# Kernel optimization log

Hardware: AMD Instinct MI355X
Metric: run time of the kernel (lower is better)

Reference implementation:

```python
import jax, jax.numpy as jnp
import numpy as np


def setup_inputs() -> dict:
    key = jax.random.key(0)
    ks = jax.random.split(key, 14)
    N, D, H, L, K = 16384, 1024, 1024, 256, 4096
    s = 0.02  # small init scale for stable activations
    return {
        "x": jax.random.uniform(ks[0], (N, D), dtype=jnp.float32),
        "embed_pool": jax.random.normal(ks[1], (K, L), dtype=jnp.float32),
        "ew1": jax.random.normal(ks[2], (D, H), dtype=jnp.float32) * s,
        "eb1": jnp.zeros((H,), jnp.float32),
        "ew2": jax.random.normal(ks[3], (H, H), dtype=jnp.float32) * s,
        "eb2": jnp.zeros((H,), jnp.float32),
        "ew3": jax.random.normal(ks[4], (H, L), dtype=jnp.float32) * s,
        "eb3": jnp.zeros((L,), jnp.float32),
        "dw1": jax.random.normal(ks[5], (L, H), dtype=jnp.float32) * s,
        "db1": jnp.zeros((H,), jnp.float32),
        "dw2": jax.random.normal(ks[6], (H, H), dtype=jnp.float32) * s,
        "db2": jnp.zeros((H,), jnp.float32),
        "dw3": jax.random.normal(ks[7], (H, D), dtype=jnp.float32) * s,
        "db3": jnp.zeros((D,), jnp.float32),
    }


def _gelu(t):
    # torch nn.GELU default = exact erf gelu
    return jax.nn.gelu(t, approximate=False)


def reference(x, embed_pool, ew1, eb1, ew2, eb2, ew3, eb3, dw1, db1, dw2, db2, dw3, db3):
    sg = jax.lax.stop_gradient
    # encoder (Dropout is identity at eval)
    h = _gelu(x @ ew1 + eb1)
    h = _gelu(h @ ew2 + eb2)
    z_e = h @ ew3 + eb3  # [N, L]
    # vectorized nearest-neighbor codebook search (argmin of ||z_e - e_k||)
    # squared distances via expansion; argmin identical to argmin of norms
    d2 = (jnp.sum(z_e * z_e, axis=1, keepdims=True)
          - 2.0 * (z_e @ embed_pool.T)
          + jnp.sum(embed_pool * embed_pool, axis=1))  # [N, K]
    z_index = jnp.argmin(d2, axis=1)  # [N]
    z_discrete = jax.nn.one_hot(z_index, embed_pool.shape[0], dtype=jnp.int32)
    z_q = embed_pool[z_index]  # [N, L]
    # straight-through estimator
    z_ss = z_e - sg(z_e) + sg(z_q)
    # decoder
    h = _gelu(z_ss @ dw1 + db1)
    h = _gelu(h @ dw2 + db2)
    x_pred = jax.nn.sigmoid(h @ dw3 + db3)  # [N, D]
    loss = (jnp.sum((x - x_pred) ** 2)
            + jnp.sum((sg(z_e) - z_q) ** 2)
            + 0.25 * jnp.sum((z_e - sg(z_q)) ** 2)) / x.shape[0]
    return x_pred, z_discrete, loss
```

## Files before the change

kernel.cpp:

```cpp
#include <hip/hip_runtime.h>
#include <math.h>


#define MB (1024ULL * 1024ULL)

typedef __attribute__((ext_vector_type(8))) short s16x8;
typedef __attribute__((ext_vector_type(4))) float f32x4;

__device__ __forceinline__ ushort f2bf(float f) {
    unsigned u = __float_as_uint(f);
    u += 0x7fffu + ((u >> 16) & 1u);
    return (ushort)(u >> 16);
}
__device__ __forceinline__ float bf2f(ushort h) {
    return __uint_as_float(((unsigned)h) << 16);
}
__device__ __forceinline__ float gelu_f(float v) {
    return 0.5f * v * (1.0f + erff(v * 0.70710678118654752f));
}
__device__ __forceinline__ void gload16(const void* g, void* l) {
    __builtin_amdgcn_global_load_lds(
        (const __attribute__((address_space(1))) void*)g,
        (__attribute__((address_space(3))) void*)l, 16, 0, 0);
}

__device__ __forceinline__ void conv_body(const float* __restrict__ in,
                                          ushort* __restrict__ out,
                                          int n8, int vb, int nB)
{
    for (int i = vb * 256 + threadIdx.x; i < n8; i += nB * 256) {
        const float4 v0 = *(const float4*)(in + (size_t)i * 8);
        const float4 v1 = *(const float4*)(in + (size_t)i * 8 + 4);
        s16x8 h;
        h[0] = f2bf(v0.x); h[1] = f2bf(v0.y); h[2] = f2bf(v0.z); h[3] = f2bf(v0.w);
        h[4] = f2bf(v1.x); h[5] = f2bf(v1.y); h[6] = f2bf(v1.z); h[7] = f2bf(v1.w);
        *(s16x8*)(out + (size_t)i * 8) = h;
    }
}

__global__ __launch_bounds__(256)
void prep_all(const float* __restrict__ x, ushort* __restrict__ xb,
              const float* __restrict__ pool, ushort* __restrict__ poolb,
              float* __restrict__ cn,
              const float* __restrict__ ew1, ushort* __restrict__ w1,
              const float* __restrict__ ew2, ushort* __restrict__ w2,
              const float* __restrict__ ew3, ushort* __restrict__ w3,
              const float* __restrict__ dw1, ushort* __restrict__ v1,
              const float* __restrict__ dw2, ushort* __restrict__ v2,
              const float* __restrict__ dw3, ushort* __restrict__ v3)
{
    __shared__ float tile[32][33];
    const int b = blockIdx.x;
    const int tid = threadIdx.x;

    if (b < 2048) {
        conv_body(x, xb, 16384 * 1024 / 8, b, 2048);
        return;
    }
    if (b < 2560) {
        conv_body(pool, poolb, 4096 * 256 / 8, b - 2048, 512);
        return;
    }
    if (b < 3584) {
        const int r = (b - 2560) * 4 + (tid >> 6);
        const int lane = tid & 63;
        float4 v = *(const float4*)(pool + (size_t)r * 256 + lane * 4);
        float s = v.x * v.x + v.y * v.y + v.z * v.z + v.w * v.w;
        #pragma unroll
        for (int o = 32; o > 0; o >>= 1) s += __shfl_down(s, o);
        if (lane == 0) cn[r] = s;
        return;
    }

    const float* in; ushort* out; int Kd, Nn, vb;
    if (b < 4608)      { in = ew1; out = w1; Kd = 1024; Nn = 1024; vb = b - 3584; }
    else if (b < 5632) { in = ew2; out = w2; Kd = 1024; Nn = 1024; vb = b - 4608; }
    else if (b < 5888) { in = ew3; out = w3; Kd = 1024; Nn = 256;  vb = b - 5632; }
    else if (b < 6144) { in = dw1; out = v1; Kd = 256;  Nn = 1024; vb = b - 5888; }
    else if (b < 7168) { in = dw2; out = v2; Kd = 1024; Nn = 1024; vb = b - 6144; }
    else               { in = dw3; out = v3; Kd = 1024; Nn = 1024; vb = b - 7168; }

    const int nxw = Nn / 32;
    const int n0 = (vb % nxw) * 32, k0 = (vb / nxw) * 32;
    const int tx = tid & 31, ty = tid >> 5;
    #pragma unroll
    for (int r = 0; r < 4; r++)
        tile[ty + r * 8][tx] = in[(size_t)(k0 + ty + r * 8) * Nn + n0 + tx];
    __syncthreads();
    #pragma unroll
    for (int r = 0; r < 4; r++) {
        const float v = tile[tx][ty + r * 8];
        out[(size_t)(n0 + ty + r * 8) * Kd + k0 + tx] = f2bf(v);
    }
}

template<int EPI>
__global__ __launch_bounds__(512, 2)
void gemm_big(const ushort* __restrict__ A, const ushort* __restrict__ B,
              const float* __restrict__ bias, int Kd, int Nn,
              ushort* __restrict__ Cu,
              float* __restrict__ pval, int* __restrict__ pidx)
{
    extern __shared__ ushort smem[];
    constexpr int BUFS = 512 * 64;

    const int tid = threadIdx.x;
    const int wave = tid >> 6, lane = tid & 63;

    const int nx = gridDim.x;
    const int nwg = nx * gridDim.y;
    const int orig = blockIdx.y * nx + blockIdx.x;
    const int wgid = (orig & 7) * (nwg >> 3) + (orig >> 3);
    const int bx = wgid % nx, by = wgid / nx;

    const int m0 = by * 256, n0 = bx * 256;
    const int wr = wave >> 2, wc = wave & 3;
    const int fcol = lane & 15, kgrp = lane >> 4;
    const int NT = Kd / 64;
    const int rs = Kd * 2;

    const int srow = lane >> 3;
    const int sswz = ((lane & 7) ^ srow) << 4;
    const char* Abase = (const char*)A + (size_t)m0 * rs;
    const char* Bbase = (const char*)B + (size_t)n0 * rs;

    f32x4 acc[8][4];
    #pragma unroll
    for (int m = 0; m < 8; m++)
        #pragma unroll
        for (int n = 0; n < 4; n++)
            acc[m][n] = (f32x4){0.f, 0.f, 0.f, 0.f};

    auto STAGE = [&](int buf, int t) {
        ushort* dst = smem + buf * BUFS;
        const size_t kb = (size_t)t * 128;
        #pragma unroll
        for (int g = 0; g < 4; g++) {
            const int rb = g * 64 + wave * 8;
            gload16(Abase + (size_t)(rb + srow) * rs + kb + sswz, dst + rb * 64);
            gload16(Bbase + (size_t)(rb + srow) * rs + kb + sswz,
                    dst + (256 + rb) * 64);
        }
    };
    auto LD = [&](int buf, int r, int u) -> s16x8 {
        return *(const s16x8*)(smem + buf * BUFS + r * 64 + ((u ^ (r & 7)) << 3));
    };

    STAGE(0, 0);
    for (int t = 0; t < NT; ++t) {
        asm volatile("s_waitcnt vmcnt(0)" ::: "memory");
        __builtin_amdgcn_s_barrier();
        if (t + 1 < NT) STAGE((t + 1) & 1, t + 1);
        const int buf = t & 1;
        s16x8 b2[4][2];
        #pragma unroll
        for (int n = 0; n < 4; n++) {
            const int r = 256 + wc * 64 + n * 16 + fcol;
            #pragma unroll
            for (int ks = 0; ks < 2; ks++) b2[n][ks] = LD(buf, r, ks * 4 + kgrp);
        }
        #pragma unroll
        for (int h = 0; h < 2; h++) {
            s16x8 a2[4][2];
            #pragma unroll
            for (int i = 0; i < 4; i++) {
                const int r = wr * 128 + (h * 4 + i) * 16 + fcol;
                #pragma unroll
                for (int ks = 0; ks < 2; ks++) a2[i][ks] = LD(buf, r, ks * 4 + kgrp);
            }
            __builtin_amdgcn_s_setprio(1);
            #pragma unroll
            for (int i = 0; i < 4; i++)
                #pragma unroll
                for (int n = 0; n < 4; n++)
                    #pragma unroll
                    for (int ks = 0; ks < 2; ks++)
                        acc[h * 4 + i][n] = __builtin_amdgcn_mfma_f32_16x16x32_bf16(
                            a2[i][ks], b2[n][ks], acc[h * 4 + i][n], 0, 0, 0);
            __builtin_amdgcn_s_setprio(0);
        }
    }
    __builtin_amdgcn_sched_barrier(0);

    int colg[4];
    float bcol[4];
    #pragma unroll
    for (int n = 0; n < 4; n++) {
        colg[n] = n0 + wc * 64 + n * 16 + fcol;
        bcol[n] = bias[colg[n]];
    }

    if constexpr (EPI == 1) {
        #pragma unroll
        for (int m = 0; m < 8; m++)
            #pragma unroll
            for (int v = 0; v < 4; v++) {
                const int row = m0 + wr * 128 + m * 16 + kgrp * 4 + v;
                #pragma unroll
                for (int n = 0; n < 4; n++) {
                    float val = gelu_f(acc[m][n][v] + bcol[n]);
                    Cu[(size_t)row * Nn + colg[n]] = f2bf(val);
                }
            }
    } else if constexpr (EPI == 3) {
        __syncthreads();
        float* sv = (float*)smem;
        int*   si = (int*)(sv + 1024);
        #pragma unroll
        for (int m = 0; m < 8; m++)
            #pragma unroll
            for (int v = 0; v < 4; v++) {
                float best = INFINITY;
                int bidx = 0x7fffffff;
                #pragma unroll
                for (int n = 0; n < 4; n++) {
                    float sc = bcol[n] - 2.0f * acc[m][n][v];
                    if (sc < best || (sc == best && colg[n] < bidx)) { best = sc; bidx = colg[n]; }
                }
                #pragma unroll
                for (int d = 1; d < 16; d <<= 1) {
                    float ov = __shfl_xor(best, d, 64);
                    int   oi = __shfl_xor(bidx, d, 64);
                    if (ov < best || (ov == best && oi < bidx)) { best = ov; bidx = oi; }
                }
                if (fcol == 0) {
                    const int rl = wr * 128 + m * 16 + kgrp * 4 + v;
                    sv[wc * 256 + rl] = best;
                    si[wc * 256 + rl] = bidx;
                }
            }
        __syncthreads();
        if (tid < 256) {
            float v0 = sv[tid];
            int   i0 = si[tid];
            #pragma unroll
            for (int c = 1; c < 4; c++) {
                float v1 = sv[c * 256 + tid];
                int   i1 = si[c * 256 + tid];
                if (v1 < v0 || (v1 == v0 && i1 < i0)) { v0 = v1; i0 = i1; }
            }
            pval[(size_t)(m0 + tid) * nx + bx] = v0;
            pidx[(size_t)(m0 + tid) * nx + bx] = i0;
        }
    }
}

template<int EPI>
__global__ __launch_bounds__(512, 2)
void gemm_128(const ushort* __restrict__ A, const ushort* __restrict__ B,
              const float* __restrict__ bias, int Kd, int Nn,
              ushort* __restrict__ Cu, float* __restrict__ Cf)
{
    extern __shared__ ushort smem[];
    constexpr int BUFS = 256 * 64;

    const int tid = threadIdx.x;
    const int wave = tid >> 6, lane = tid & 63;

    const int nx = gridDim.x;
    const int nwg = nx * gridDim.y;
    const int orig = blockIdx.y * nx + blockIdx.x;
    const int wgid = (orig & 7) * (nwg >> 3) + (orig >> 3);
    const int bx = wgid % nx, by = wgid / nx;

    const int m0 = by * 128, n0 = bx * 128;
    const int wr = wave >> 2, wc = wave & 3;
    const int fcol = lane & 15, kgrp = lane >> 4;
    const int NT = Kd / 64;
    const int rs = Kd * 2;

    const int srow = lane >> 3;
    const int sswz = ((lane & 7) ^ srow) << 4;
    const char* Abase = (const char*)A + (size_t)m0 * rs;
    const char* Bbase = (const char*)B + (size_t)n0 * rs;

    f32x4 acc[4][2];
    #pragma unroll
    for (int m = 0; m < 4; m++)
        #pragma unroll
        for (int n = 0; n < 2; n++)
            acc[m][n] = (f32x4){0.f, 0.f, 0.f, 0.f};

    auto STAGE = [&](int buf, int t) {
        ushort* dst = smem + buf * BUFS;
        const size_t kb = (size_t)t * 128;
        #pragma unroll
        for (int g = 0; g < 2; g++) {
            const int rb = g * 64 + wave * 8;
            gload16(Abase + (size_t)(rb + srow) * rs + kb + sswz, dst + rb * 64);
            gload16(Bbase + (size_t)(rb + srow) * rs + kb + sswz,
                    dst + (128 + rb) * 64);
        }
    };
    auto LD = [&](int buf, int r, int u) -> s16x8 {
        return *(const s16x8*)(smem + buf * BUFS + r * 64 + ((u ^ (r & 7)) << 3));
    };

    STAGE(0, 0);
    STAGE(1, 1);
    for (int t = 0; t < NT; ++t) {
        if (t + 1 < NT) asm volatile("s_waitcnt vmcnt(4)" ::: "memory");
        else            asm volatile("s_waitcnt vmcnt(0)" ::: "memory");
        __builtin_amdgcn_s_barrier();
        if (t + 2 < NT) STAGE((t + 2) % 3, t + 2);
        const int buf = t % 3;
        s16x8 a2[4][2], b2[2][2];
        #pragma unroll
        for (int m = 0; m < 4; m++) {
            const int r = wr * 64 + m * 16 + fcol;
            #pragma unroll
            for (int ks = 0; ks < 2; ks++) a2[m][ks] = LD(buf, r, ks * 4 + kgrp);
        }
        #pragma unroll
        for (int n = 0; n < 2; n++) {
            const int r = 128 + wc * 32 + n * 16 + fcol;
            #pragma unroll
            for (int ks = 0; ks < 2; ks++) b2[n][ks] = LD(buf, r, ks * 4 + kgrp);
        }
        __builtin_amdgcn_s_setprio(1);
        #pragma unroll
        for (int m = 0; m < 4; m++)
            #pragma unroll
            for (int n = 0; n < 2; n++)
                #pragma unroll
                for (int ks = 0; ks < 2; ks++)
                    acc[m][n] = __builtin_amdgcn_mfma_f32_16x16x32_bf16(
                        a2[m][ks], b2[n][ks], acc[m][n], 0, 0, 0);
        __builtin_amdgcn_s_setprio(0);
    }
    __builtin_amdgcn_sched_barrier(0);

    #pragma unroll
    for (int n = 0; n < 2; n++) {
        const int col = n0 + wc * 32 + n * 16 + fcol;
        const float bc = bias[col];
        #pragma unroll
        for (int m = 0; m < 4; m++)
            #pragma unroll
            for (int v = 0; v < 4; v++) {
                const int row = m0 + wr * 64 + m * 16 + kgrp * 4 + v;
                float val = acc[m][n][v] + bc;
                if constexpr (EPI == 0) {
                    Cu[(size_t)row * Nn + col] = f2bf(val);
                } else if constexpr (EPI == 1) {
                    Cu[(size_t)row * Nn + col] = f2bf(gelu_f(val));
                } else {
                    Cf[(size_t)row * Nn + col] = 1.0f / (1.0f + expf(-val));
                }
            }
    }
}

__global__ __launch_bounds__(256)
void argmin_final(const float* __restrict__ pval, const int* __restrict__ pidx,
                  int nblk, const ushort* __restrict__ zE,
                  const float* __restrict__ pool,
                  float* __restrict__ zdisc, int* __restrict__ kbo,
                  float* __restrict__ vqP)
{
    const int t = threadIdx.x;
    const int r = blockIdx.x * 4 + (t >> 6);
    const int l = t & 63;

    float best = INFINITY;
    int bi = 0x7fffffff;
    if (l < nblk) {
        best = pval[(size_t)r * nblk + l];
        bi = pidx[(size_t)r * nblk + l];
    }
    #pragma unroll
    for (int d = 32; d > 0; d >>= 1) {
        float ov = __shfl_xor(best, d, 64);
        int   oi = __shfl_xor(bi, d, 64);
        if (ov < best || (ov == best && oi < bi)) { best = ov; bi = oi; }
    }
    const int kbest = bi;

    f32x4* zrow = (f32x4*)(zdisc + (size_t)r * 4096);
    #pragma unroll
    for (int it = 0; it < 16; it++) {
        const int j = it * 64 + l;
        f32x4 o = (f32x4){0.f, 0.f, 0.f, 0.f};
        if ((kbest >> 2) == j) o[kbest & 3] = 1.0f;
        __builtin_nontemporal_store(o, &zrow[j]);
    }

    const float4 pz = *(const float4*)(pool + (size_t)kbest * 256 + l * 4);
    const ushort4 zh = *(const ushort4*)(zE + (size_t)r * 256 + l * 4);
    float d0 = bf2f(zh.x) - pz.x;
    float d1 = bf2f(zh.y) - pz.y;
    float d2 = bf2f(zh.z) - pz.z;
    float d3 = bf2f(zh.w) - pz.w;
    float s = d0 * d0 + d1 * d1 + d2 * d2 + d3 * d3;
    #pragma unroll
    for (int o = 32; o > 0; o >>= 1) s += __shfl_xor(s, o, 64);
    if (l == 0) { vqP[r] = s; kbo[r] = kbest; }
}

__global__ __launch_bounds__(256)
void gather_pred(const int* __restrict__ kb, const float* __restrict__ xpT,
                 const float* __restrict__ x, float* __restrict__ xpred,
                 float* __restrict__ sseP)
{
    const int t = threadIdx.x;
    const int r = blockIdx.x * 4 + (t >> 6);
    const int l = t & 63;
    const int k = kb[r];
    const float* src = xpT + (size_t)k * 1024;
    const float* xr  = x + (size_t)r * 1024;
    float* dst = xpred + (size_t)r * 1024;
    float s = 0.0f;
    #pragma unroll
    for (int j = 0; j < 4; j++) {
        const int c = (j * 64 + l) * 4;
        f32x4 v = *(const f32x4*)(src + c);
        const float4 xv = *(const float4*)(xr + c);
        __builtin_nontemporal_store(v, (f32x4*)(dst + c));
        float d0 = xv.x - v[0], d1 = xv.y - v[1];
        float d2 = xv.z - v[2], d3 = xv.w - v[3];
        s += d0 * d0 + d1 * d1 + d2 * d2 + d3 * d3;
    }
    #pragma unroll
    for (int o = 32; o > 0; o >>= 1) s += __shfl_xor(s, o, 64);
    if (l == 0) sseP[r] = s;
}

__global__ __launch_bounds__(256)
void loss_final(const float* __restrict__ sseP, int nP,
                const float* __restrict__ vqP, int nV,
                float* __restrict__ out)
{
    int tid = threadIdx.x;
    float sx = 0.0f, svq = 0.0f;
    for (int i = tid; i < nP; i += 256) sx += sseP[i];
    for (int i = tid; i < nV; i += 256) svq += vqP[i];
    __shared__ float a[256], b[256];
    a[tid] = sx; b[tid] = svq;
    __syncthreads();
    for (int s = 128; s > 0; s >>= 1) {
        if (tid < s) { a[tid] += a[tid + s]; b[tid] += b[tid + s]; }
        __syncthreads();
    }
    if (tid == 0) out[0] = (a[0] + 1.25f * b[0]) / 16384.0f;
}

extern "C" void kernel_launch(void* const* d_in, const int* in_sizes, int n_in,
                              void* d_out, int out_size, void* d_ws, size_t ws_size,
                              hipStream_t stream)
{
    const float* x    = (const float*)d_in[0];
    const float* pool = (const float*)d_in[1];
    const float* ew1  = (const float*)d_in[2];
    const float* eb1  = (const float*)d_in[3];
    const float* ew2  = (const float*)d_in[4];
    const float* eb2  = (const float*)d_in[5];
    const float* ew3  = (const float*)d_in[6];
    const float* eb3  = (const float*)d_in[7];
    const float* dw1  = (const float*)d_in[8];
    const float* db1  = (const float*)d_in[9];
    const float* dw2  = (const float*)d_in[10];
    const float* db2  = (const float*)d_in[11];
    const float* dw3  = (const float*)d_in[12];
    const float* db3  = (const float*)d_in[13];

    const int N = 16384, D = 1024, H = 1024, L = 256, K = 4096;

    float* out   = (float*)d_out;
    float* xpred = out;
    float* zdisc = out + (size_t)N * D;
    float* lossp = zdisc + (size_t)N * K;

    char* ws = (char*)d_ws;
    ushort* xb    = (ushort*)(ws + 0 * MB);
    ushort* h1    = (ushort*)(ws + 32 * MB);
    ushort* h2    = (ushort*)(ws + 64 * MB);
    ushort* zE    = (ushort*)(ws + 96 * MB);
    ushort* poolb = (ushort*)(ws + 104 * MB);
    ushort* w1    = (ushort*)(ws + 106 * MB);
    ushort* w2    = (ushort*)(ws + 108 * MB);
    ushort* w3    = (ushort*)(ws + 110 * MB);
    ushort* v1    = (ushort*)(ws + 111 * MB);
    ushort* v2    = (ushort*)(ws + 112 * MB);
    ushort* v3    = (ushort*)(ws + 114 * MB);
    ushort* t3    = (ushort*)(ws + 116 * MB);
    ushort* t4    = (ushort*)(ws + 124 * MB);
    float*  xpT   = (float*)(ws + 132 * MB);
    float*  cn    = (float*)(ws + 148 * MB);
    float*  pv    = (float*)(ws + 149 * MB);
    int*    pi    = (int*)(ws + 150 * MB);
    int*    kbo   = (int*)(ws + 151 * MB);
    float*  vqP   = (float*)(ws + 152 * MB);
    float*  sxP   = (float*)(ws + 153 * MB);

    const int SH_BIG = 2 * (512 * 64) * 2;
    const int SH_128 = 3 * (256 * 64) * 2;
    (void)hipFuncSetAttribute((const void*)gemm_big<1>,
        hipFuncAttributeMaxDynamicSharedMemorySize, SH_BIG);
    (void)hipFuncSetAttribute((const void*)gemm_big<3>,
        hipFuncAttributeMaxDynamicSharedMemorySize, SH_BIG);
    (void)hipFuncSetAttribute((const void*)gemm_128<0>,
        hipFuncAttributeMaxDynamicSharedMemorySize, SH_128);
    (void)hipFuncSetAttribute((const void*)gemm_128<1>,
        hipFuncAttributeMaxDynamicSharedMemorySize, SH_128);
    (void)hipFuncSetAttribute((const void*)gemm_128<2>,
        hipFuncAttributeMaxDynamicSharedMemorySize, SH_128);

    dim3 blk(256), gblk(512);

    prep_all<<<8192, blk, 0, stream>>>(x, xb, pool, poolb, cn,
                                       ew1, w1, ew2, w2, ew3, w3,
                                       dw1, v1, dw2, v2, dw3, v3);

    gemm_128<1><<<dim3(H / 128, K / 128), gblk, SH_128, stream>>>(
        poolb, v1, db1, L, H, t3, nullptr);
    gemm_128<1><<<dim3(H / 128, K / 128), gblk, SH_128, stream>>>(
        t3, v2, db2, H, H, t4, nullptr);
    gemm_128<2><<<dim3(D / 128, K / 128), gblk, SH_128, stream>>>(
        t4, v3, db3, H, D, nullptr, xpT);

    gemm_big<1><<<dim3(H / 256, N / 256), gblk, SH_BIG, stream>>>(
        xb, w1, eb1, D, H, h1, nullptr, nullptr);
    gemm_big<1><<<dim3(H / 256, N / 256), gblk, SH_BIG, stream>>>(
        h1, w2, eb2, H, H, h2, nullptr, nullptr);
    gemm_128<0><<<dim3(L / 128, N / 128), gblk, SH_128, stream>>>(
        h2, w3, eb3, H, L, zE, nullptr);

    gemm_big<3><<<dim3(K / 256, N / 256), gblk, SH_BIG, stream>>>(
        zE, poolb, cn, L, K, nullptr, pv, pi);

    argmin_final<<<N / 4, blk, 0, stream>>>(pv, pi, K / 256, zE, pool, zdisc, kbo, vqP);

    gather_pred<<<N / 4, blk, 0, stream>>>(kbo, xpT, x, xpred, sxP);

    loss_final<<<1, blk, 0, stream>>>(sxP, N, vqP, N, lossp);
}
```

Before: 370.7 us.

## Zero one-hot output inside distance GEMM and fuse argmin with prediction gather

The distance GEMM epilogue now writes zeros to its 256x256 tile of the one-hot output, so the argmin kernel only needs to store a single 1.0 per row. The argmin kernel and the prediction-gather kernel are merged into one launch that reuses the chosen index directly, which drops the intermediate index buffer and one kernel launch. The cost is extra store traffic in the GEMM epilogue, and correctness now relies on the zeroing store finishing before the single-element write in the next kernel, which stream ordering provides.

```diff
diff --git a/kernel.cpp b/kernel.cpp
--- a/kernel.cpp
+++ b/kernel.cpp
@@ -99,7 +99,8 @@
 void gemm_big(const ushort* __restrict__ A, const ushort* __restrict__ B,
               const float* __restrict__ bias, int Kd, int Nn,
               ushort* __restrict__ Cu,
-              float* __restrict__ pval, int* __restrict__ pidx)
+              float* __restrict__ pval, int* __restrict__ pidx,
+              float* __restrict__ zd)
 {
     extern __shared__ ushort smem[];
     constexpr int BUFS = 512 * 64;
@@ -242,6 +243,14 @@
             pval[(size_t)(m0 + tid) * nx + bx] = v0;
             pidx[(size_t)(m0 + tid) * nx + bx] = i0;
         }
+        const int lrow = tid >> 6;
+        const int cseg = (tid & 63) * 4;
+        const f32x4 z4 = (f32x4){0.f, 0.f, 0.f, 0.f};
+        #pragma unroll
+        for (int p = 0; p < 32; p++) {
+            float* zp = zd + (size_t)(m0 + p * 8 + lrow) * Nn + n0 + cseg;
+            __builtin_nontemporal_store(z4, (f32x4*)zp);
+        }
     }
 }
 
@@ -352,11 +361,13 @@
 }
 
 __global__ __launch_bounds__(256)
-void argmin_final(const float* __restrict__ pval, const int* __restrict__ pidx,
-                  int nblk, const ushort* __restrict__ zE,
-                  const float* __restrict__ pool,
-                  float* __restrict__ zdisc, int* __restrict__ kbo,
-                  float* __restrict__ vqP)
+void argmin_gather(const float* __restrict__ pval, const int* __restrict__ pidx,
+                   int nblk, const ushort* __restrict__ zE,
+                   const float* __restrict__ pool,
+                   float* __restrict__ zdisc,
+                   const float* __restrict__ xpT, const float* __restrict__ x,
+                   float* __restrict__ xpred,
+                   float* __restrict__ vqP, float* __restrict__ sseP)
 {
     const int t = threadIdx.x;
     const int r = blockIdx.x * 4 + (t >> 6);
@@ -376,14 +387,7 @@
     }
     const int kbest = bi;
 
-    f32x4* zrow = (f32x4*)(zdisc + (size_t)r * 4096);
-    #pragma unroll
-    for (int it = 0; it < 16; it++) {
-        const int j = it * 64 + l;
-        f32x4 o = (f32x4){0.f, 0.f, 0.f, 0.f};
-        if ((kbest >> 2) == j) o[kbest & 3] = 1.0f;
-        __builtin_nontemporal_store(o, &zrow[j]);
-    }
+    if (l == 0) zdisc[(size_t)r * 4096 + kbest] = 1.0f;
 
     const float4 pz = *(const float4*)(pool + (size_t)kbest * 256 + l * 4);
     const ushort4 zh = *(const ushort4*)(zE + (size_t)r * 256 + l * 4);
@@ -391,22 +395,9 @@
     float d1 = bf2f(zh.y) - pz.y;
     float d2 = bf2f(zh.z) - pz.z;
     float d3 = bf2f(zh.w) - pz.w;
-    float s = d0 * d0 + d1 * d1 + d2 * d2 + d3 * d3;
-    #pragma unroll
-    for (int o = 32; o > 0; o >>= 1) s += __shfl_xor(s, o, 64);
-    if (l == 0) { vqP[r] = s; kbo[r] = kbest; }
-}
-
-__global__ __launch_bounds__(256)
-void gather_pred(const int* __restrict__ kb, const float* __restrict__ xpT,
-                 const float* __restrict__ x, float* __restrict__ xpred,
-                 float* __restrict__ sseP)
-{
-    const int t = threadIdx.x;
-    const int r = blockIdx.x * 4 + (t >> 6);
-    const int l = t & 63;
-    const int k = kb[r];
-    const float* src = xpT + (size_t)k * 1024;
+    float svq = d0 * d0 + d1 * d1 + d2 * d2 + d3 * d3;
+
+    const float* src = xpT + (size_t)kbest * 1024;
     const float* xr  = x + (size_t)r * 1024;
     float* dst = xpred + (size_t)r * 1024;
     float s = 0.0f;
@@ -416,13 +407,16 @@
         f32x4 v = *(const f32x4*)(src + c);
         const float4 xv = *(const float4*)(xr + c);
         __builtin_nontemporal_store(v, (f32x4*)(dst + c));
-        float d0 = xv.x - v[0], d1 = xv.y - v[1];
-        float d2 = xv.z - v[2], d3 = xv.w - v[3];
-        s += d0 * d0 + d1 * d1 + d2 * d2 + d3 * d3;
-    }
-    #pragma unroll
-    for (int o = 32; o > 0; o >>= 1) s += __shfl_xor(s, o, 64);
-    if (l == 0) sseP[r] = s;
+        float e0 = xv.x - v[0], e1 = xv.y - v[1];
+        float e2 = xv.z - v[2], e3 = xv.w - v[3];
+        s += e0 * e0 + e1 * e1 + e2 * e2 + e3 * e3;
+    }
+    #pragma unroll
+    for (int o = 32; o > 0; o >>= 1) {
+        s   += __shfl_xor(s, o, 64);
+        svq += __shfl_xor(svq, o, 64);
+    }
+    if (l == 0) { sseP[r] = s; vqP[r] = svq; }
 }
 
 __global__ __launch_bounds__(256)
@@ -488,9 +482,8 @@
     float*  cn    = (float*)(ws + 148 * MB);
     float*  pv    = (float*)(ws + 149 * MB);
     int*    pi    = (int*)(ws + 150 * MB);
-    int*    kbo   = (int*)(ws + 151 * MB);
-    float*  vqP   = (float*)(ws + 152 * MB);
-    float*  sxP   = (float*)(ws + 153 * MB);
+    float*  vqP   = (float*)(ws + 151 * MB);
+    float*  sxP   = (float*)(ws + 152 * MB);
 
     const int SH_BIG = 2 * (512 * 64) * 2;
     const int SH_128 = 3 * (256 * 64) * 2;
@@ -519,18 +512,17 @@
         t4, v3, db3, H, D, nullptr, xpT);
 
     gemm_big<1><<<dim3(H / 256, N / 256), gblk, SH_BIG, stream>>>(
-        xb, w1, eb1, D, H, h1, nullptr, nullptr);
+        xb, w1, eb1, D, H, h1, nullptr, nullptr, nullptr);
     gemm_big<1><<<dim3(H / 256, N / 256), gblk, SH_BIG, stream>>>(
-        h1, w2, eb2, H, H, h2, nullptr, nullptr);
+        h1, w2, eb2, H, H, h2, nullptr, nullptr, nullptr);
     gemm_128<0><<<dim3(L / 128, N / 128), gblk, SH_128, stream>>>(
         h2, w3, eb3, H, L, zE, nullptr);
 
     gemm_big<3><<<dim3(K / 256, N / 256), gblk, SH_BIG, stream>>>(
-        zE, poolb, cn, L, K, nullptr, pv, pi);
-
-    argmin_final<<<N / 4, blk, 0, stream>>>(pv, pi, K / 256, zE, pool, zdisc, kbo, vqP);
-
-    gather_pred<<<N / 4, blk, 0, stream>>>(kbo, xpT, x, xpred, sxP);
+        zE, poolb, cn, L, K, nullptr, pv, pi, zdisc);
+
+    argmin_gather<<<N / 4, blk, 0, stream>>>(pv, pi, K / 256, zE, pool,
+                                             zdisc, xpT, x, xpred, vqP, sxP);
 
     loss_final<<<1, blk, 0, stream>>>(sxP, N, vqP, N, lossp);
 }
```

New measurement: 353.5 us. 1.05x faster.
